# Performance work log

Measured on AMD Instinct MI355X. Metric: run time of the kernel, lower is better.

Reference implementation:

```python
import jax, jax.numpy as jnp
import numpy as np

EPS = 1e-8

def setup_inputs() -> dict:
    key = jax.random.key(0)
    ks = jax.random.split(key, 4)
    B, N, D = 16, 2048, 1024
    APP = 1024
    x = jax.random.normal(ks[0], (B, N, D), dtype=jnp.float32)
    mask = jax.random.uniform(ks[1], (N, B), dtype=jnp.float32)  # [N, B] per original
    Wp = jax.random.normal(ks[2], (1024, D), dtype=jnp.float32) * 0.02
    bp = jnp.zeros((1024,), dtype=jnp.float32)
    Wv = jax.random.normal(ks[3], (APP, D), dtype=jnp.float32) * 0.02
    bv = jnp.zeros((APP,), dtype=jnp.float32)
    return {"x": x, "mask": mask, "Wp": Wp, "bp": bp, "Wv": Wv, "bv": bv}

def reference(x, mask, Wp, bp, Wv, bv):
    # proj + ReLU: [B,N,1024]
    xp = jax.nn.relu(jnp.einsum('bnd,pd->bnp', x, Wp) + bp)
    # L2-normalize along feature dim (matches xp / (norm + eps))
    xp = xp / (jnp.linalg.norm(xp, axis=2, keepdims=True) + EPS)
    # mask: [N,B] -> [B,N] (transpose+reshape in original yields [B,1,N])
    m = mask.T  # [B, N]
    # att_i = sum_j m_j * <xp_i, xp_j> / sum_j m_j  == <xp_i, sum_j m_j xp_j> / sum_j m_j
    ws = jnp.einsum('bn,bnp->bp', m, xp)                # [B, 1024]
    att = jnp.einsum('bnp,bp->bn', xp, ws) / jnp.sum(m, axis=1, keepdims=True)  # [B, N]
    # value + ReLU: [B,N,APP]
    xv = jax.nn.relu(jnp.einsum('bnd,ad->bna', x, Wv) + bv)
    return att[:, :, None] * xv
```

## Files before the change

kernel.cpp:

```cpp
#include <hip/hip_runtime.h>

#define B_  16
#define N_  2048
#define D_  1024
#define P_  1024
#define M_  (B_*N_)

typedef __attribute__((ext_vector_type(8))) short bf16x8;
typedef __attribute__((ext_vector_type(4))) float f32x4;

__device__ __forceinline__ float bf2f(unsigned short u) {
    union { unsigned int i; float f; } v; v.i = ((unsigned int)u) << 16; return v.f;
}
__device__ __forceinline__ unsigned short f2bf(float f) {
    union { unsigned int i; float f; } v; v.f = f;
    unsigned int i = v.i;
    return (unsigned short)((i + 0x7FFFu + ((i >> 16) & 1u)) >> 16);
}

__device__ __forceinline__ void async_cp16(const void* g, void* s) {
    __builtin_amdgcn_global_load_lds((const __attribute__((address_space(1))) void*)g,
                                     (__attribute__((address_space(3))) void*)s,
                                     16, 0, 0);
}

__global__ void cvt_all_k(const float* __restrict__ x,  unsigned short* __restrict__ xb,
                          const float* __restrict__ Wp, unsigned short* __restrict__ Wpb,
                          const float* __restrict__ Wv, unsigned short* __restrict__ Wvb)
{
    const int stride = gridDim.x * 256 * 4;
    const int base = (blockIdx.x * 256 + threadIdx.x) * 4;
    for (int i = base; i < M_ * D_; i += stride) {
        float4 v = *(const float4*)(x + i);
        union { unsigned short u[4]; unsigned long long ll; } p;
        p.u[0]=f2bf(v.x); p.u[1]=f2bf(v.y); p.u[2]=f2bf(v.z); p.u[3]=f2bf(v.w);
        *(unsigned long long*)(xb + i) = p.ll;
    }
    for (int i = base; i < P_ * D_; i += stride) {
        float4 v = *(const float4*)(Wp + i);
        union { unsigned short u[4]; unsigned long long ll; } p;
        p.u[0]=f2bf(v.x); p.u[1]=f2bf(v.y); p.u[2]=f2bf(v.z); p.u[3]=f2bf(v.w);
        *(unsigned long long*)(Wpb + i) = p.ll;
    }
    for (int i = base; i < P_ * D_; i += stride) {
        float4 v = *(const float4*)(Wv + i);
        union { unsigned short u[4]; unsigned long long ll; } p;
        p.u[0]=f2bf(v.x); p.u[1]=f2bf(v.y); p.u[2]=f2bf(v.z); p.u[3]=f2bf(v.w);
        *(unsigned long long*)(Wvb + i) = p.ll;
    }
}

template<int MODE>
__global__ __launch_bounds__(512, 2) void gemm8p(const unsigned short* __restrict__ A,
                                                 const unsigned short* __restrict__ W,
                                                 const float* __restrict__ bias,
                                                 const float* __restrict__ att,
                                                 void* __restrict__ Cv)
{
    __shared__ unsigned short smem[65536];

    const int id  = blockIdx.x;
    const int xcd = id & 7, idx = id >> 3;
    const int bx  = idx & 3;
    const int by  = xcd * 16 + (idx >> 2);
    const int m0  = by << 8, p0 = bx << 8;

    const int t    = threadIdx.x;
    const int lane = t & 63, wave = t >> 6;
    const int wr   = wave >> 2, wc = wave & 3;
    const int lr   = lane & 15, lq = lane >> 4;

    const int aBase = (wr * 64 + lr) * 64;
    const int bBase = (wc * 32 + lr) * 64;
    const int c0 = ((lq       ^ (lr & 7)) & 7) * 8;
    const int c1 = (((lq | 4) ^ (lr & 7)) & 7) * 8;

    const int srowT = t >> 3;
    const int slot8 = (t & 7) * 8;
    const int lch8  = (((t & 7) ^ (srowT & 7)) & 7) * 8;
    const unsigned short* Ag = A + ((size_t)m0 << 10) + lch8;
    const unsigned short* Bg = W + ((size_t)p0 << 10) + lch8;

    auto stageA = [&](int buf, int rb, int tt) {
        const unsigned short* s = Ag + ((size_t)(rb + srowT) << 10) + (tt << 6);
        async_cp16(s,                      smem + buf * 16384 + (rb + srowT) * 64 + slot8);
        async_cp16(s + ((size_t)64 << 10), smem + buf * 16384 + (rb + 64 + srowT) * 64 + slot8);
    };
    auto stageB = [&](int buf, int rb, int tt) {
        const unsigned short* s = Bg + ((size_t)(rb + srowT) << 10) + (tt << 6);
        async_cp16(s,                      smem + 32768 + buf * 16384 + (rb + srowT) * 64 + slot8);
        async_cp16(s + ((size_t)64 << 10), smem + 32768 + buf * 16384 + (rb + 64 + srowT) * 64 + slot8);
    };

    f32x4 acc[8][4];
    #pragma unroll
    for (int i = 0; i < 8; ++i)
        #pragma unroll
        for (int j = 0; j < 4; ++j) acc[i][j] = (f32x4){0.f, 0.f, 0.f, 0.f};

    bf16x8 aR[2][4][2];
    bf16x8 bR[2][2][2];

#define RD_A(BUF, MH) do {                                                            \
    const unsigned short* Ab_ = smem + (BUF) * 16384 + (MH) * 8192 + aBase;           \
    _Pragma("unroll")                                                                 \
    for (int i_ = 0; i_ < 4; ++i_) {                                                  \
        aR[MH][i_][0] = *(const bf16x8*)(Ab_ + i_ * 1024 + c0);                       \
        aR[MH][i_][1] = *(const bf16x8*)(Ab_ + i_ * 1024 + c1);                       \
    } } while (0)

#define RD_B(BUF, NH) do {                                                            \
    const unsigned short* Bb_ = smem + 32768 + (BUF) * 16384 + (NH) * 8192 + bBase;   \
    _Pragma("unroll")                                                                 \
    for (int j_ = 0; j_ < 2; ++j_) {                                                  \
        bR[NH][j_][0] = *(const bf16x8*)(Bb_ + j_ * 1024 + c0);                       \
        bR[NH][j_][1] = *(const bf16x8*)(Bb_ + j_ * 1024 + c1);                       \
    } } while (0)

#define MM(MH, NH) do {                                                               \
    __builtin_amdgcn_s_setprio(1);                                                    \
    _Pragma("unroll")                                                                 \
    for (int h_ = 0; h_ < 2; ++h_)                                                    \
        _Pragma("unroll")                                                             \
        for (int i_ = 0; i_ < 4; ++i_)                                                \
            _Pragma("unroll")                                                         \
            for (int j_ = 0; j_ < 2; ++j_)                                            \
                acc[(MH) * 4 + i_][(NH) * 2 + j_] =                                   \
                    __builtin_amdgcn_mfma_f32_16x16x32_bf16(                          \
                        aR[MH][i_][h_], bR[NH][j_][h_],                               \
                        acc[(MH) * 4 + i_][(NH) * 2 + j_], 0, 0, 0);                  \
    __builtin_amdgcn_s_setprio(0); } while (0)

#define LGKM(N) do { asm volatile("s_waitcnt lgkmcnt(" #N ")" ::: "memory");          \
                     __builtin_amdgcn_sched_barrier(0); } while (0)
#define VMC(N)  do { asm volatile("s_waitcnt vmcnt(" #N ")" ::: "memory");            \
                     __builtin_amdgcn_sched_barrier(0); } while (0)
#define BAR()   __builtin_amdgcn_s_barrier()

    stageA(0, 0, 0); stageB(0, 0, 0); stageA(0, 128, 0); stageB(0, 128, 0);
    stageA(1, 0, 1); stageB(1, 0, 1); stageA(1, 128, 1); stageB(1, 128, 1);
    VMC(8);
    BAR();
    RD_A(0, 0);
    RD_B(0, 0);

    #pragma unroll 1
    for (int it = 0; it < 8; ++it) {
        const int t1 = 2 * it + 1;
        const int t2 = (2 * it + 2) & 15;
        const int t3 = (2 * it + 3) & 15;
        RD_A(0, 1); stageB(1, 128, t1);
        BAR(); LGKM(8); MM(0, 0); BAR();
        RD_B(0, 1); stageA(1, 128, t1);
        BAR(); LGKM(4); MM(1, 0); BAR();
        stageA(0, 0, t2);
        BAR(); LGKM(0); MM(1, 1); VMC(6); BAR();
        stageB(0, 0, t2);
        BAR(); LGKM(0); MM(0, 1);
        RD_A(1, 0); RD_B(1, 0);
        VMC(4); BAR();
        RD_A(1, 1); stageB(0, 128, t2);
        BAR(); LGKM(8); MM(0, 0); BAR();
        RD_B(1, 1); stageA(0, 128, t2);
        BAR(); LGKM(4); MM(1, 0); BAR();
        stageA(1, 0, t3);
        BAR(); LGKM(0); MM(1, 1); VMC(6); BAR();
        stageB(1, 0, t3);
        BAR(); LGKM(0); MM(0, 1);
        RD_A(0, 0); RD_B(0, 0);
        VMC(4); BAR();
    }
#undef RD_A
#undef RD_B
#undef MM
#undef LGKM
#undef VMC
#undef BAR

    asm volatile("s_waitcnt vmcnt(0) lgkmcnt(0)" ::: "memory");
    __syncthreads();

    if (MODE == 0) {
        float bi[4];
        #pragma unroll
        for (int nj = 0; nj < 4; ++nj)
            bi[nj] = bias[p0 + ((nj >> 1) << 7) + wc * 32 + ((nj & 1) << 4) + lr];
        unsigned short* Cp = (unsigned short*)Cv;
        #pragma unroll
        for (int mh = 0; mh < 2; ++mh) {
            #pragma unroll
            for (int i = 0; i < 4; ++i) {
                const int rl = wr * 64 + i * 16 + lq * 4;
                #pragma unroll
                for (int nj = 0; nj < 4; ++nj) {
                    const int colL = ((nj >> 1) << 7) + wc * 32 + ((nj & 1) << 4) + lr;
                    #pragma unroll
                    for (int v = 0; v < 4; ++v) {
                        const float val = fmaxf(acc[mh * 4 + i][nj][v] + bi[nj], 0.f);
                        smem[(rl + v) * 256 + colL] = f2bf(val);
                    }
                }
            }
            __syncthreads();
            #pragma unroll
            for (int pas = 0; pas < 8; ++pas) {
                const int ix = pas * 512 + t;
                const int row = ix >> 5, ch = ix & 31;
                bf16x8 vv = *(const bf16x8*)(smem + row * 256 + ch * 8);
                *(bf16x8*)(Cp + (size_t)(m0 + mh * 128 + row) * P_ + p0 + ch * 8) = vv;
            }
            __syncthreads();
        }
    } else {
        float* Cp = (float*)Cv;
        #pragma unroll
        for (int mi = 0; mi < 8; ++mi) {
            const int row = m0 + ((mi >> 2) << 7) + wr * 64 + ((mi & 3) << 4) + lq * 4;
            float av[4];
            #pragma unroll
            for (int v = 0; v < 4; ++v) av[v] = att[row + v];
            #pragma unroll
            for (int nj = 0; nj < 4; ++nj) {
                const int col = p0 + ((nj >> 1) << 7) + wc * 32 + ((nj & 1) << 4) + lr;
                const float b0v = bias[col];
                #pragma unroll
                for (int v = 0; v < 4; ++v) {
                    const float val = fmaxf(acc[mi][nj][v] + b0v, 0.f);
                    Cp[(size_t)(row + v) * P_ + col] = val * av[v];
                }
            }
        }
    }
}

template<int MODE>
__global__ __launch_bounds__(256) void gemm_f32(const float* __restrict__ A,
                                                const float* __restrict__ W,
                                                const float* __restrict__ bias,
                                                const float* __restrict__ att,
                                                void* __restrict__ Cv)
{
    const int K = D_, BK = 32;
    __shared__ float As[128 * 32];
    __shared__ float Bs[128 * 32];
    const int id = blockIdx.x;
    const int bx = (id >> 3) & 7;
    const int by = ((id >> 6) << 3) | (id & 7);
    const int m0 = by * 128, p0 = bx * 128;
    const int wave = threadIdx.x >> 6, lane = threadIdx.x & 63;
    const int wr = wave >> 1, wc = wave & 1;
    const int srow = wave * 32 + (lane >> 3);
    const int scol = (lane & 7) * 4;
    const float* ag = A + (size_t)(m0 + srow) * K + scol;
    const float* bg = W + (size_t)(p0 + srow) * K + scol;
    float* as = &As[srow * BK + scol];
    float* bs = &Bs[srow * BK + scol];
    f32x4 acc[4][4];
    #pragma unroll
    for (int i = 0; i < 4; i++)
        #pragma unroll
        for (int j = 0; j < 4; j++) acc[i][j] = (f32x4){0.f,0.f,0.f,0.f};
    const int lr = lane & 15, lq = lane >> 4;
    const float* Ar = &As[(wr * 64 + lr) * BK + lq * 8];
    const float* Br = &Bs[(wc * 64 + lr) * BK + lq * 8];
    for (int kb = 0; kb < K; kb += BK) {
        #pragma unroll
        for (int s = 0; s < 4; s++) {
            async_cp16(ag + (size_t)s * 8 * K + kb, as + s * 8 * BK);
            async_cp16(bg + (size_t)s * 8 * K + kb, bs + s * 8 * BK);
        }
        __syncthreads();
        bf16x8 af[4], bf[4];
        #pragma unroll
        for (int i = 0; i < 4; i++) {
            f32x4 a0 = *(const f32x4*)(Ar + i * 16 * BK);
            f32x4 a1 = *(const f32x4*)(Ar + i * 16 * BK + 4);
            #pragma unroll
            for (int e = 0; e < 4; e++) {
                union { float f; unsigned int u; } c;
                c.f = a0[e]; af[i][e]     = (short)(c.u >> 16);
                c.f = a1[e]; af[i][e + 4] = (short)(c.u >> 16);
            }
        }
        #pragma unroll
        for (int j = 0; j < 4; j++) {
            f32x4 b0 = *(const f32x4*)(Br + j * 16 * BK);
            f32x4 b1 = *(const f32x4*)(Br + j * 16 * BK + 4);
            #pragma unroll
            for (int e = 0; e < 4; e++) {
                union { float f; unsigned int u; } c;
                c.f = b0[e]; bf[j][e]     = (short)(c.u >> 16);
                c.f = b1[e]; bf[j][e + 4] = (short)(c.u >> 16);
            }
        }
        #pragma unroll
        for (int i = 0; i < 4; i++)
            #pragma unroll
            for (int j = 0; j < 4; j++)
                acc[i][j] = __builtin_amdgcn_mfma_f32_16x16x32_bf16(af[i], bf[j], acc[i][j], 0, 0, 0);
        __syncthreads();
    }
    const int crow0 = m0 + wr * 64 + lq * 4;
    const int ccol0 = p0 + wc * 64 + lr;
    #pragma unroll
    for (int i = 0; i < 4; i++) {
        float attv[4];
        if (MODE == 1) {
            #pragma unroll
            for (int v = 0; v < 4; v++) attv[v] = att[crow0 + i * 16 + v];
        }
        #pragma unroll
        for (int j = 0; j < 4; j++) {
            const int col = ccol0 + j * 16;
            const float bi = bias[col];
            #pragma unroll
            for (int v = 0; v < 4; v++) {
                const int row = crow0 + i * 16 + v;
                float val = fmaxf(acc[i][j][v] + bi, 0.0f);
                if (MODE == 0) ((unsigned short*)Cv)[(size_t)row * P_ + col] = f2bf(val);
                else           ((float*)Cv)[(size_t)row * P_ + col] = val * attv[v];
            }
        }
    }
}

__global__ __launch_bounds__(256) void fused_nc_k(const unsigned short* __restrict__ X1,
                                                  const float* __restrict__ mask,
                                                  float* __restrict__ inv,
                                                  float* __restrict__ wsv,
                                                  float* __restrict__ msum)
{
    __shared__ float accw[4][1024];
    __shared__ float mred[4];
    const int b = blockIdx.y, nc = blockIdx.x;
    const int wave = threadIdx.x >> 6, lane = threadIdx.x & 63;
    float acc[16];
    #pragma unroll
    for (int e = 0; e < 16; e++) acc[e] = 0.f;
    float msub = 0.f;
    const int rbase = b * N_ + nc * 32 + wave * 8;
    const int nbase = nc * 32 + wave * 8;
    for (int t = 0; t < 8; t++) {
        const int r = rbase + t;
        const unsigned short* row = X1 + (size_t)r * P_;
        bf16x8 u0 = *(const bf16x8*)(row + lane * 16);
        bf16x8 u1 = *(const bf16x8*)(row + lane * 16 + 8);
        float v[16], s = 0.f;
        #pragma unroll
        for (int e = 0; e < 8; e++) { v[e] = bf2f((unsigned short)u0[e]); s += v[e]*v[e]; }
        #pragma unroll
        for (int e = 0; e < 8; e++) { v[8+e] = bf2f((unsigned short)u1[e]); s += v[8+e]*v[8+e]; }
        #pragma unroll
        for (int off = 32; off > 0; off >>= 1) s += __shfl_down(s, off);
        s = __shfl(s, 0);
        const float iv = 1.f / (sqrtf(s) + 1e-8f);
        const float mk = mask[(nbase + t) * B_ + b];
        if (lane == 0) { inv[r] = iv; msub += mk; }
        const float w = mk * iv;
        #pragma unroll
        for (int e = 0; e < 16; e++) acc[e] += w * v[e];
    }
    #pragma unroll
    for (int e = 0; e < 16; e++) accw[wave][e * 64 + lane] = acc[e];
    if (lane == 0) mred[wave] = msub;
    __syncthreads();
    #pragma unroll
    for (int q = 0; q < 4; q++) {
        const int p = threadIdx.x * 4 + q;
        const int col = (p & 63) * 16 + (p >> 6);
        float ssum = accw[0][p] + accw[1][p] + accw[2][p] + accw[3][p];
        atomicAdd(&wsv[b * P_ + col], ssum);
    }
    if (threadIdx.x == 0) atomicAdd(&msum[b], mred[0] + mred[1] + mred[2] + mred[3]);
}

__global__ void att_k(const unsigned short* __restrict__ X1,
                      const float* __restrict__ wsvec,
                      const float* __restrict__ inv,
                      const float* __restrict__ msum,
                      float* __restrict__ att)
{
    const int r = blockIdx.x * 4 + (threadIdx.x >> 6);
    const int lane = threadIdx.x & 63;
    const int b = r >> 11;
    const unsigned short* row = X1 + (size_t)r * P_;
    const float* w = wsvec + b * P_;
    bf16x8 u0 = *(const bf16x8*)(row + lane * 8);
    bf16x8 u1 = *(const bf16x8*)(row + 512 + lane * 8);
    f32x4 w0 = *(const f32x4*)(w + lane * 8);
    f32x4 w1 = *(const f32x4*)(w + lane * 8 + 4);
    f32x4 w2 = *(const f32x4*)(w + 512 + lane * 8);
    f32x4 w3 = *(const f32x4*)(w + 512 + lane * 8 + 4);
    float s = 0.f;
    #pragma unroll
    for (int k = 0; k < 4; k++) s += bf2f((unsigned short)u0[k]) * w0[k];
    #pragma unroll
    for (int k = 0; k < 4; k++) s += bf2f((unsigned short)u0[k + 4]) * w1[k];
    #pragma unroll
    for (int k = 0; k < 4; k++) s += bf2f((unsigned short)u1[k]) * w2[k];
    #pragma unroll
    for (int k = 0; k < 4; k++) s += bf2f((unsigned short)u1[k + 4]) * w3[k];
    #pragma unroll
    for (int off = 32; off > 0; off >>= 1) s += __shfl_down(s, off);
    if (lane == 0) att[r] = s * inv[r] / msum[b];
}

extern "C" void kernel_launch(void* const* d_in, const int* in_sizes, int n_in,
                              void* d_out, int out_size, void* d_ws, size_t ws_size,
                              hipStream_t stream)
{
    const float* x    = (const float*)d_in[0];
    const float* mask = (const float*)d_in[1];
    const float* Wp   = (const float*)d_in[2];
    const float* bp   = (const float*)d_in[3];
    const float* Wv   = (const float*)d_in[4];
    const float* bv   = (const float*)d_in[5];
    float* out = (float*)d_out;

    unsigned short* X1 = (unsigned short*)d_out;

    const size_t xb_bytes = (size_t)M_ * D_ * 2;
    const size_t wb_bytes = (size_t)P_ * D_ * 2;
    const size_t f_bytes  = 2 * (size_t)M_ * 4 + (size_t)B_ * P_ * 4 + 64;
    const bool big_ws = ws_size >= xb_bytes + 2 * wb_bytes + f_bytes;

    char* ws = (char*)d_ws;
    size_t off = 0;
    unsigned short *xb = nullptr, *Wpb = nullptr, *Wvb = nullptr;
    if (big_ws) {
        xb  = (unsigned short*)(ws + off); off += xb_bytes;
        Wpb = (unsigned short*)(ws + off); off += wb_bytes;
        Wvb = (unsigned short*)(ws + off); off += wb_bytes;
    }
    float* inv  = (float*)(ws + off); off += (size_t)M_ * 4;
    float* att  = (float*)(ws + off); off += (size_t)M_ * 4;
    float* wsv  = (float*)(ws + off); off += (size_t)B_ * P_ * 4;
    float* msum = (float*)(ws + off); off += 64;

    hipMemsetAsync(wsv, 0, (size_t)B_ * P_ * 4 + 64, stream);

    if (big_ws) {
        cvt_all_k<<<2048, 256, 0, stream>>>(x, xb, Wp, Wpb, Wv, Wvb);
        gemm8p<0><<<512, 512, 0, stream>>>(xb, Wpb, bp, nullptr, X1);
    } else {
        const int gblocks = (P_ / 128) * (M_ / 128);
        gemm_f32<0><<<gblocks, 256, 0, stream>>>(x, Wp, bp, nullptr, X1);
    }
    fused_nc_k<<<dim3(64, B_), 256, 0, stream>>>(X1, mask, inv, wsv, msum);
    att_k<<<M_ / 4, 256, 0, stream>>>(X1, wsv, inv, msum, att);
    if (big_ws) gemm8p<1><<<512, 512, 0, stream>>>(xb, Wvb, bv, att, out);
    else {
        const int gblocks = (P_ / 128) * (M_ / 128);
        gemm_f32<1><<<gblocks, 256, 0, stream>>>(x, Wv, bv, att, out);
    }
}
```

Baseline: 414.2 us.

## Compute two N-tiles per GEMM block with overlapped epilogue and chunked C staging

```diff
diff --git a/kernel.cpp b/kernel.cpp
--- a/kernel.cpp
+++ b/kernel.cpp
@@ -58,12 +58,14 @@
                                                  void* __restrict__ Cv)
 {
     __shared__ unsigned short smem[65536];
+    __shared__ unsigned short cbuf[8192];
 
     const int id  = blockIdx.x;
     const int xcd = id & 7, idx = id >> 3;
-    const int bx  = idx & 3;
-    const int by  = xcd * 16 + (idx >> 2);
-    const int m0  = by << 8, p0 = bx << 8;
+    const int bz  = idx & 1;
+    const int by  = xcd * 16 + (idx >> 1);
+    const int m0  = by << 8;
+    const int p0  = (bz * 2) << 8;
 
     const int t    = threadIdx.x;
     const int lane = t & 63, wave = t >> 6;
@@ -79,15 +81,16 @@
     const int slot8 = (t & 7) * 8;
     const int lch8  = (((t & 7) ^ (srowT & 7)) & 7) * 8;
     const unsigned short* Ag = A + ((size_t)m0 << 10) + lch8;
-    const unsigned short* Bg = W + ((size_t)p0 << 10) + lch8;
+    const unsigned short* Bg = W + lch8;
 
     auto stageA = [&](int buf, int rb, int tt) {
-        const unsigned short* s = Ag + ((size_t)(rb + srowT) << 10) + (tt << 6);
+        const unsigned short* s = Ag + ((size_t)(rb + srowT) << 10) + ((tt & 15) << 6);
         async_cp16(s,                      smem + buf * 16384 + (rb + srowT) * 64 + slot8);
         async_cp16(s + ((size_t)64 << 10), smem + buf * 16384 + (rb + 64 + srowT) * 64 + slot8);
     };
     auto stageB = [&](int buf, int rb, int tt) {
-        const unsigned short* s = Bg + ((size_t)(rb + srowT) << 10) + (tt << 6);
+        const int prow = p0 + ((tt >> 4) << 8) + rb + srowT;
+        const unsigned short* s = Bg + ((size_t)prow << 10) + ((tt & 15) << 6);
         async_cp16(s,                      smem + 32768 + buf * 16384 + (rb + srowT) * 64 + slot8);
         async_cp16(s + ((size_t)64 << 10), smem + 32768 + buf * 16384 + (rb + 64 + srowT) * 64 + slot8);
     };
@@ -100,6 +103,66 @@
 
     bf16x8 aR[2][4][2];
     bf16x8 bR[2][2][2];
+
+    auto writeC = [&](int tile) {
+        const int p0t = p0 + (tile << 8);
+        if (MODE == 0) {
+            float bi[4];
+            #pragma unroll
+            for (int nj = 0; nj < 4; ++nj)
+                bi[nj] = bias[p0t + ((nj >> 1) << 7) + wc * 32 + ((nj & 1) << 4) + lr];
+            unsigned short* Cp = (unsigned short*)Cv;
+            #pragma unroll 1
+            for (int w = 0; w < 8; ++w) {
+                const int mh = w >> 2, wsel = (w >> 1) & 1, i0 = (w & 1) * 2;
+                if (wr == wsel) {
+                    #pragma unroll
+                    for (int ib = 0; ib < 2; ++ib) {
+                        const int i = i0 + ib;
+                        #pragma unroll
+                        for (int nj = 0; nj < 4; ++nj) {
+                            const int colL = ((nj >> 1) << 7) + wc * 32 + ((nj & 1) << 4) + lr;
+                            #pragma unroll
+                            for (int v = 0; v < 4; ++v) {
+                                const float val = fmaxf(acc[mh * 4 + i][nj][v] + bi[nj], 0.f);
+                                cbuf[(ib * 16 + lq * 4 + v) * 256 + colL] = f2bf(val);
+                            }
+                        }
+                    }
+                }
+                asm volatile("s_waitcnt lgkmcnt(0)" ::: "memory");
+                __builtin_amdgcn_s_barrier();
+                #pragma unroll
+                for (int q = 0; q < 2; ++q) {
+                    const int ix = q * 512 + t;
+                    const int r = ix >> 5, ch = ix & 31;
+                    bf16x8 vv = *(const bf16x8*)(cbuf + r * 256 + ch * 8);
+                    *(bf16x8*)(Cp + (size_t)(m0 + w * 32 + r) * P_ + p0t + ch * 8) = vv;
+                }
+                __builtin_amdgcn_sched_barrier(0);
+                __builtin_amdgcn_s_barrier();
+            }
+        } else {
+            float* Cp = (float*)Cv;
+            #pragma unroll
+            for (int mi = 0; mi < 8; ++mi) {
+                const int row = m0 + ((mi >> 2) << 7) + wr * 64 + ((mi & 3) << 4) + lq * 4;
+                float av[4];
+                #pragma unroll
+                for (int v = 0; v < 4; ++v) av[v] = att[row + v];
+                #pragma unroll
+                for (int nj = 0; nj < 4; ++nj) {
+                    const int col = p0t + ((nj >> 1) << 7) + wc * 32 + ((nj & 1) << 4) + lr;
+                    const float b0v = bias[col];
+                    #pragma unroll
+                    for (int v = 0; v < 4; ++v) {
+                        const float val = fmaxf(acc[mi][nj][v] + b0v, 0.f);
+                        Cp[(size_t)(row + v) * P_ + col] = val * av[v];
+                    }
+                }
+            }
+        }
+    };
 
 #define RD_A(BUF, MH) do {                                                            \
     const unsigned short* Ab_ = smem + (BUF) * 16384 + (MH) * 8192 + aBase;           \
@@ -145,13 +208,13 @@
     RD_B(0, 0);
 
     #pragma unroll 1
-    for (int it = 0; it < 8; ++it) {
+    for (int it = 0; it < 16; ++it) {
         const int t1 = 2 * it + 1;
-        const int t2 = (2 * it + 2) & 15;
-        const int t3 = (2 * it + 3) & 15;
-        RD_A(0, 1); stageB(1, 128, t1);
+        const int t2 = (2 * it + 2) & 31;
+        const int t3 = (2 * it + 3) & 31;
+        RD_A(0, 1); if (it) stageB(1, 128, t1);
         BAR(); LGKM(8); MM(0, 0); BAR();
-        RD_B(0, 1); stageA(1, 128, t1);
+        RD_B(0, 1); if (it) stageA(1, 128, t1);
         BAR(); LGKM(4); MM(1, 0); BAR();
         stageA(0, 0, t2);
         BAR(); LGKM(0); MM(1, 1); VMC(6); BAR();
@@ -169,6 +232,13 @@
         BAR(); LGKM(0); MM(0, 1);
         RD_A(0, 0); RD_B(0, 0);
         VMC(4); BAR();
+        if (it == 7) {
+            writeC(0);
+            #pragma unroll
+            for (int i = 0; i < 8; ++i)
+                #pragma unroll
+                for (int j = 0; j < 4; ++j) acc[i][j] = (f32x4){0.f, 0.f, 0.f, 0.f};
+        }
     }
 #undef RD_A
 #undef RD_B
@@ -178,59 +248,8 @@
 #undef BAR
 
     asm volatile("s_waitcnt vmcnt(0) lgkmcnt(0)" ::: "memory");
-    __syncthreads();
-
-    if (MODE == 0) {
-        float bi[4];
-        #pragma unroll
-        for (int nj = 0; nj < 4; ++nj)
-            bi[nj] = bias[p0 + ((nj >> 1) << 7) + wc * 32 + ((nj & 1) << 4) + lr];
-        unsigned short* Cp = (unsigned short*)Cv;
-        #pragma unroll
-        for (int mh = 0; mh < 2; ++mh) {
-            #pragma unroll
-            for (int i = 0; i < 4; ++i) {
-                const int rl = wr * 64 + i * 16 + lq * 4;
-                #pragma unroll
-                for (int nj = 0; nj < 4; ++nj) {
-                    const int colL = ((nj >> 1) << 7) + wc * 32 + ((nj & 1) << 4) + lr;
-                    #pragma unroll
-                    for (int v = 0; v < 4; ++v) {
-                        const float val = fmaxf(acc[mh * 4 + i][nj][v] + bi[nj], 0.f);
-                        smem[(rl + v) * 256 + colL] = f2bf(val);
-                    }
-                }
-            }
-            __syncthreads();
-            #pragma unroll
-            for (int pas = 0; pas < 8; ++pas) {
-                const int ix = pas * 512 + t;
-                const int row = ix >> 5, ch = ix & 31;
-                bf16x8 vv = *(const bf16x8*)(smem + row * 256 + ch * 8);
-                *(bf16x8*)(Cp + (size_t)(m0 + mh * 128 + row) * P_ + p0 + ch * 8) = vv;
-            }
-            __syncthreads();
-        }
-    } else {
-        float* Cp = (float*)Cv;
-        #pragma unroll
-        for (int mi = 0; mi < 8; ++mi) {
-            const int row = m0 + ((mi >> 2) << 7) + wr * 64 + ((mi & 3) << 4) + lq * 4;
-            float av[4];
-            #pragma unroll
-            for (int v = 0; v < 4; ++v) av[v] = att[row + v];
-            #pragma unroll
-            for (int nj = 0; nj < 4; ++nj) {
-                const int col = p0 + ((nj >> 1) << 7) + wc * 32 + ((nj & 1) << 4) + lr;
-                const float b0v = bias[col];
-                #pragma unroll
-                for (int v = 0; v < 4; ++v) {
-                    const float val = fmaxf(acc[mi][nj][v] + b0v, 0.f);
-                    Cp[(size_t)(row + v) * P_ + col] = val * av[v];
-                }
-            }
-        }
-    }
+    __builtin_amdgcn_s_barrier();
+    writeC(1);
 }
 
 template<int MODE>
@@ -441,14 +460,14 @@
 
     if (big_ws) {
         cvt_all_k<<<2048, 256, 0, stream>>>(x, xb, Wp, Wpb, Wv, Wvb);
-        gemm8p<0><<<512, 512, 0, stream>>>(xb, Wpb, bp, nullptr, X1);
+        gemm8p<0><<<256, 512, 0, stream>>>(xb, Wpb, bp, nullptr, X1);
     } else {
         const int gblocks = (P_ / 128) * (M_ / 128);
         gemm_f32<0><<<gblocks, 256, 0, stream>>>(x, Wp, bp, nullptr, X1);
     }
     fused_nc_k<<<dim3(64, B_), 256, 0, stream>>>(X1, mask, inv, wsv, msum);
     att_k<<<M_ / 4, 256, 0, stream>>>(X1, wsv, inv, msum, att);
-    if (big_ws) gemm8p<1><<<512, 512, 0, stream>>>(xb, Wvb, bv, att, out);
+    if (big_ws) gemm8p<1><<<256, 512, 0, stream>>>(xb, Wvb, bv, att, out);
     else {
         const int gblocks = (P_ / 128) * (M_ / 128);
         gemm_f32<1><<<gblocks, 256, 0, stream>>>(x, Wv, bv, att, out);
```

Result: slower. 762.3 us (+84.0%).
